# Performance work log

Hardware: AMD Instinct MI355X
Metric: run time of the kernel (lower is better)

Reference implementation:

```python
import jax, jax.numpy as jnp
import numpy as np

PROCESSING_STEPS = 3


def setup_inputs() -> dict:
    key = jax.random.key(0)
    ks = jax.random.split(key, 8)
    B, N, d = 1024, 128, 128
    y = jax.random.normal(ks[0], (B, N, d), dtype=jnp.float32)
    lengths = jax.random.randint(ks[1], (B,), 1, N + 1, dtype=jnp.int32)
    s = 0.05
    W_ih = jax.random.normal(ks[2], (4 * d, 2 * d), dtype=jnp.float32) * s
    W_hh = jax.random.normal(ks[3], (4 * d, d), dtype=jnp.float32) * s
    b_ih = jax.random.normal(ks[4], (4 * d,), dtype=jnp.float32) * s
    b_hh = jax.random.normal(ks[5], (4 * d,), dtype=jnp.float32) * s
    W_m = jax.random.normal(ks[6], (1, 2 * d), dtype=jnp.float32) * s
    b_m = jax.random.normal(ks[7], (1,), dtype=jnp.float32) * s
    mean = jnp.zeros((1,), jnp.float32)
    stddev = jnp.ones((1,), jnp.float32)
    return {"y": y, "lengths": lengths, "W_ih": W_ih, "W_hh": W_hh,
            "b_ih": b_ih, "b_hh": b_hh, "W_m": W_m, "b_m": b_m,
            "mean": mean, "stddev": stddev}


def reference(y, lengths, W_ih, W_hh, b_ih, b_hh, W_m, b_m, mean, stddev):
    # y: [B, N, d] padded atomwise representation; lengths: valid atoms per molecule
    B, N, d = y.shape
    mask = jnp.arange(N)[None, :] < lengths[:, None]          # [B, N]
    maskf = mask.astype(y.dtype)[..., None]                    # [B, N, 1]
    neg_inf = jnp.finfo(y.dtype).min

    q_star = jnp.zeros((B, 2 * d), y.dtype)
    h = jnp.zeros((B, d), y.dtype)
    c = jnp.zeros((B, d), y.dtype)

    def step(carry, _):
        q_star, h, c = carry
        # single-layer LSTM cell (PyTorch gate order i, f, g, o)
        gates = q_star @ W_ih.T + b_ih + h @ W_hh.T + b_hh     # [B, 4d]
        i, f, g, o = jnp.split(gates, 4, axis=-1)
        c2 = jax.nn.sigmoid(f) * c + jax.nn.sigmoid(i) * jnp.tanh(g)
        h2 = jax.nn.sigmoid(o) * jnp.tanh(c2)
        q = h2                                                  # [B, d]
        # attention: gather q per atom, segment softmax, scatter_add
        e = jnp.einsum('bnd,bd->bn', y, q)                      # [B, N]
        e = jnp.where(mask, e, neg_inf)
        a = jax.nn.softmax(e, axis=-1)[..., None] * maskf       # [B, N, 1]
        r = jnp.sum(a * y, axis=1)                              # [B, d]
        return (jnp.concatenate([q, r], axis=-1), h2, c2), None

    (q_star, h, c), _ = jax.lax.scan(step, (q_star, h, c), None,
                                     length=PROCESSING_STEPS)
    out = q_star @ W_m.T + b_m                                  # [B, 1]
    return out * stddev + mean
```

## Files before the change

### kernel.cpp

```cpp
#include <hip/hip_runtime.h>
#include <math.h>

#define BB 1024
#define NN 128
#define DD 128

__device__ __forceinline__ float fsig_(float x)  { return 1.0f / (1.0f + __expf(-x)); }
__device__ __forceinline__ float ftanh_(float x) { return 2.0f / (1.0f + __expf(-2.0f * x)) - 1.0f; }

__global__ __launch_bounds__(256) void k_prep2(
    const float* __restrict__ W_ih, const float* __restrict__ W_hh,
    const float* __restrict__ b_ih, const float* __restrict__ b_hh,
    float* __restrict__ Wfull, float* __restrict__ gbase) {
  int b = blockIdx.x, t = threadIdx.x;
  if (b < 64) {
    int base = b * 2048;
    for (int i = t; i < 2048; i += 256) {
      int idx = base + i;
      int j = idx >> 8, d = idx & 255;
      float v = W_ih[(j << 8) + d];
      if (d < 128) v += W_hh[(j << 7) + d];
      Wfull[idx] = v;
    }
  } else {
    __shared__ float h1l[DD];
    if (t < DD) {
      float bi = b_ih[t] + b_hh[t];
      float bg = b_ih[256 + t] + b_hh[256 + t];
      float bo = b_ih[384 + t] + b_hh[384 + t];
      float cc = fsig_(bi) * ftanh_(bg);
      h1l[t] = fsig_(bo) * ftanh_(cc);
    }
    __syncthreads();
    int j0 = (b - 64) * 128;
    if (t < 128) {
      int j = j0 + t;
      float acc = b_ih[j] + b_hh[j];
      #pragma unroll 8
      for (int d = 0; d < DD; ++d)
        acc = fmaf(W_ih[(j << 8) + d] + W_hh[(j << 7) + d], h1l[d], acc);
      gbase[j] = acc;
    }
  }
}

struct SMX {
  float ql[DD];
  float c1l[DD];
  float rp[4][DD];
  float xcat[256];
  float g2[512];
  float c2l[DD];
  float reds[4], redf[4];
};

__global__ __launch_bounds__(256, 4) void k_fused(
    const float* __restrict__ y, const int* __restrict__ lengths,
    const float* __restrict__ Wfull, const float* __restrict__ gbase,
    const float* __restrict__ b_ih, const float* __restrict__ b_hh,
    const float* __restrict__ Wm, const float* __restrict__ bm,
    const float* __restrict__ mn, const float* __restrict__ sd,
    float* __restrict__ out) {
  __shared__ SMX s;
  const int t = threadIdx.x;
  const int lane = t & 63, w = t >> 6;
  const int sub = lane & 15, g = lane >> 4;
  const int d0 = sub << 3;
  const int wbase = w << 2;
  const int m = blockIdx.x;
  const int len = lengths[m];
  const float* yb = y + (size_t)m * (NN * DD);

  if (t < DD) {
    float bi = b_ih[t] + b_hh[t];
    float bg = b_ih[256 + t] + b_hh[256 + t];
    float bo = b_ih[384 + t] + b_hh[384 + t];
    float cc = fsig_(bi) * ftanh_(bg);
    s.c1l[t] = cc;
    s.ql[t] = fsig_(bo) * ftanh_(cc);
  }

  float4 va[8], vb[8];
  #pragma unroll
  for (int it = 0; it < 8; ++it) {
    int n = (it << 4) + wbase + g;
    int nc = (n < len) ? n : (len - 1);
    const float4* yr = (const float4*)(yb + nc * DD + d0);
    va[it] = yr[0];
    vb[it] = yr[1];
  }
  __syncthreads();

  auto attn = [&](bool is_final) {
    float4 q0 = *(const float4*)&s.ql[d0];
    float4 q1 = *(const float4*)&s.ql[d0 + 4];
    float a[8], sl = 0.0f;
    #pragma unroll
    for (int it = 0; it < 8; ++it) {
      int nw = (it << 4) + wbase;
      if (nw < len) {
        int n = nw + g;
        float p = fmaf(va[it].x, q0.x, fmaf(va[it].y, q0.y,
                  fmaf(va[it].z, q0.z, fmaf(va[it].w, q0.w,
                  fmaf(vb[it].x, q1.x, fmaf(vb[it].y, q1.y,
                  fmaf(vb[it].z, q1.z, vb[it].w * q1.w)))))));
        #pragma unroll
        for (int sh = 1; sh < 16; sh <<= 1) p += __shfl_xor(p, sh, 64);
        a[it] = (n < len) ? __expf(p) : 0.0f;
      } else {
        a[it] = 0.0f;
      }
      sl += a[it];
    }
    #pragma unroll
    for (int sh = 1; sh < 64; sh <<= 1) sl += __shfl_xor(sl, sh, 64);
    if (lane == 0) s.reds[w] = sl;
    __syncthreads();
    float wscale = 16.0f / (s.reds[0] + s.reds[1] + s.reds[2] + s.reds[3]);

    float4 r0 = {0.f, 0.f, 0.f, 0.f}, r1 = {0.f, 0.f, 0.f, 0.f};
    #pragma unroll
    for (int it = 0; it < 8; ++it) {
      int nw = (it << 4) + wbase;
      if (nw < len) {
        float av = a[it];
        r0.x = fmaf(av, va[it].x, r0.x); r0.y = fmaf(av, va[it].y, r0.y);
        r0.z = fmaf(av, va[it].z, r0.z); r0.w = fmaf(av, va[it].w, r0.w);
        r1.x = fmaf(av, vb[it].x, r1.x); r1.y = fmaf(av, vb[it].y, r1.y);
        r1.z = fmaf(av, vb[it].z, r1.z); r1.w = fmaf(av, vb[it].w, r1.w);
      }
    }
    r0.x *= wscale; r0.y *= wscale; r0.z *= wscale; r0.w *= wscale;
    r1.x *= wscale; r1.y *= wscale; r1.z *= wscale; r1.w *= wscale;
    #pragma unroll
    for (int sh = 16; sh < 64; sh <<= 1) {
      r0.x += __shfl_xor(r0.x, sh, 64); r0.y += __shfl_xor(r0.y, sh, 64);
      r0.z += __shfl_xor(r0.z, sh, 64); r0.w += __shfl_xor(r0.w, sh, 64);
      r1.x += __shfl_xor(r1.x, sh, 64); r1.y += __shfl_xor(r1.y, sh, 64);
      r1.z += __shfl_xor(r1.z, sh, 64); r1.w += __shfl_xor(r1.w, sh, 64);
    }
    if (g == 0) {
      *(float4*)&s.rp[w][d0] = r0;
      *(float4*)&s.rp[w][d0 + 4] = r1;
    }
    __syncthreads();
    if (!is_final) {
      if (t < DD) s.xcat[128 + t] = s.rp[0][t] + s.rp[1][t] + s.rp[2][t] + s.rp[3][t];
      __syncthreads();
    } else {
      float part = 0.0f;
      if (t < DD) {
        float r_ = s.rp[0][t] + s.rp[1][t] + s.rp[2][t] + s.rp[3][t];
        part = Wm[t] * s.ql[t] + Wm[DD + t] * r_;
      }
      #pragma unroll
      for (int sh = 1; sh < 64; sh <<= 1) part += __shfl_xor(part, sh, 64);
      if (lane == 0) s.redf[w] = part;
      __syncthreads();
      if (t == 0)
        out[m] = (s.redf[0] + s.redf[1] + s.redf[2] + s.redf[3] + bm[0]) * sd[0] + mn[0];
    }
  };

  auto matvec = [&](int qlo, const float* bias_g, bool use_gbase) {
    #pragma unroll 4
    for (int iter = 0; iter < 32; ++iter) {
      int j = (iter << 4) + wbase + g;
      const float4* wr = (const float4*)(Wfull + (j << 8));
      float acc = 0.0f;
      #pragma unroll
      for (int q = 0; q < 4; ++q) {
        if (q < qlo) continue;
        int idx = (q << 4) + sub;
        float4 wv = wr[idx];
        float4 xa = *(const float4*)&s.xcat[idx << 2];
        acc = fmaf(wv.x, xa.x, fmaf(wv.y, xa.y, fmaf(wv.z, xa.z, fmaf(wv.w, xa.w, acc))));
      }
      #pragma unroll
      for (int sh = 1; sh < 16; sh <<= 1) acc += __shfl_xor(acc, sh, 64);
      if (sub == 0)
        s.g2[j] = acc + (use_gbase ? bias_g[j] : (b_ih[j] + b_hh[j]));
    }
  };

  auto nonlin = [&](const float* cin_src, bool save_c) {
    if (t < DD) {
      float I = s.g2[t], F = s.g2[128 + t];
      float G = s.g2[256 + t], O = s.g2[384 + t];
      float cc = fmaf(fsig_(F), cin_src[t], fsig_(I) * ftanh_(G));
      float hh = fsig_(O) * ftanh_(cc);
      if (save_c) s.c2l[t] = cc;
      s.xcat[t] = hh;
      s.ql[t] = hh;
    }
    __syncthreads();
  };

  attn(false);
  matvec(2, gbase, true);
  __syncthreads();
  nonlin(s.c1l, true);
  attn(false);
  matvec(0, nullptr, false);
  __syncthreads();
  nonlin(s.c2l, false);
  attn(true);
}

extern "C" void kernel_launch(void* const* d_in, const int* in_sizes, int n_in,
                              void* d_out, int out_size, void* d_ws, size_t ws_size,
                              hipStream_t stream) {
  const float* y    = (const float*)d_in[0];
  const int*   len  = (const int*)  d_in[1];
  const float* W_ih = (const float*)d_in[2];
  const float* W_hh = (const float*)d_in[3];
  const float* b_ih = (const float*)d_in[4];
  const float* b_hh = (const float*)d_in[5];
  const float* W_m  = (const float*)d_in[6];
  const float* b_m  = (const float*)d_in[7];
  const float* mean = (const float*)d_in[8];
  const float* sd   = (const float*)d_in[9];
  float* out = (float*)d_out;

  float* ws    = (float*)d_ws;
  float* Wfull = ws;
  float* gbase = ws + 131072;

  k_prep2<<<68, 256, 0, stream>>>(W_ih, W_hh, b_ih, b_hh, Wfull, gbase);
  k_fused<<<BB, 256, 0, stream>>>(y, len, Wfull, gbase, b_ih, b_hh,
                                  W_m, b_m, mean, sd, out);
}
```

Measured before the change: 74.99 us.

## Store fused LSTM weights as bf16 and use 512-thread blocks

The prep kernel now writes the combined LSTM weight matrix in bf16 rounding instead of fp32, halving the bytes each block streams for the gate matvec. The main kernel moves from 256 to 512 threads per block, so each wave holds fewer atom rows in registers and each thread does half the matvec rows. Reductions over waves are widened to 8 partials. This trades accuracy in the gate computation for less weight bandwidth and more parallelism per molecule.

```diff
diff --git a/kernel.cpp b/kernel.cpp
--- a/kernel.cpp
+++ b/kernel.cpp
@@ -7,11 +7,18 @@
 
 __device__ __forceinline__ float fsig_(float x)  { return 1.0f / (1.0f + __expf(-x)); }
 __device__ __forceinline__ float ftanh_(float x) { return 2.0f / (1.0f + __expf(-2.0f * x)) - 1.0f; }
-
-__global__ __launch_bounds__(256) void k_prep2(
+__device__ __forceinline__ unsigned short to_bf16_(float f) {
+  unsigned u = __float_as_uint(f);
+  u = (u + 0x7FFFu + ((u >> 16) & 1u)) >> 16;
+  return (unsigned short)u;
+}
+__device__ __forceinline__ float bf16_lo_(unsigned u) { return __uint_as_float(u << 16); }
+__device__ __forceinline__ float bf16_hi_(unsigned u) { return __uint_as_float(u & 0xFFFF0000u); }
+
+__global__ __launch_bounds__(256) void k_prep3(
     const float* __restrict__ W_ih, const float* __restrict__ W_hh,
     const float* __restrict__ b_ih, const float* __restrict__ b_hh,
-    float* __restrict__ Wfull, float* __restrict__ gbase) {
+    unsigned short* __restrict__ Wbf, float* __restrict__ gbase) {
   int b = blockIdx.x, t = threadIdx.x;
   if (b < 64) {
     int base = b * 2048;
@@ -20,7 +27,7 @@
       int j = idx >> 8, d = idx & 255;
       float v = W_ih[(j << 8) + d];
       if (d < 128) v += W_hh[(j << 7) + d];
-      Wfull[idx] = v;
+      Wbf[idx] = to_bf16_(v);
     }
   } else {
     __shared__ float h1l[DD];
@@ -47,16 +54,16 @@
 struct SMX {
   float ql[DD];
   float c1l[DD];
-  float rp[4][DD];
+  float rp[8][DD];
   float xcat[256];
   float g2[512];
   float c2l[DD];
-  float reds[4], redf[4];
+  float reds[8], redf[2];
 };
 
-__global__ __launch_bounds__(256, 4) void k_fused(
+__global__ __launch_bounds__(512, 8) void k_fused(
     const float* __restrict__ y, const int* __restrict__ lengths,
-    const float* __restrict__ Wfull, const float* __restrict__ gbase,
+    const unsigned short* __restrict__ Wbf, const float* __restrict__ gbase,
     const float* __restrict__ b_ih, const float* __restrict__ b_hh,
     const float* __restrict__ Wm, const float* __restrict__ bm,
     const float* __restrict__ mn, const float* __restrict__ sd,
@@ -66,7 +73,6 @@
   const int lane = t & 63, w = t >> 6;
   const int sub = lane & 15, g = lane >> 4;
   const int d0 = sub << 3;
-  const int wbase = w << 2;
   const int m = blockIdx.x;
   const int len = lengths[m];
   const float* yb = y + (size_t)m * (NN * DD);
@@ -80,10 +86,10 @@
     s.ql[t] = fsig_(bo) * ftanh_(cc);
   }
 
-  float4 va[8], vb[8];
+  float4 va[4], vb[4];
   #pragma unroll
-  for (int it = 0; it < 8; ++it) {
-    int n = (it << 4) + wbase + g;
+  for (int it = 0; it < 4; ++it) {
+    int n = (it << 5) + (w << 2) + g;
     int nc = (n < len) ? n : (len - 1);
     const float4* yr = (const float4*)(yb + nc * DD + d0);
     va[it] = yr[0];
@@ -94,10 +100,10 @@
   auto attn = [&](bool is_final) {
     float4 q0 = *(const float4*)&s.ql[d0];
     float4 q1 = *(const float4*)&s.ql[d0 + 4];
-    float a[8], sl = 0.0f;
-    #pragma unroll
-    for (int it = 0; it < 8; ++it) {
-      int nw = (it << 4) + wbase;
+    float a[4], sl = 0.0f;
+    #pragma unroll
+    for (int it = 0; it < 4; ++it) {
+      int nw = (it << 5) + (w << 2);
       if (nw < len) {
         int n = nw + g;
         float p = fmaf(va[it].x, q0.x, fmaf(va[it].y, q0.y,
@@ -116,12 +122,14 @@
     for (int sh = 1; sh < 64; sh <<= 1) sl += __shfl_xor(sl, sh, 64);
     if (lane == 0) s.reds[w] = sl;
     __syncthreads();
-    float wscale = 16.0f / (s.reds[0] + s.reds[1] + s.reds[2] + s.reds[3]);
+    float Z = s.reds[0] + s.reds[1] + s.reds[2] + s.reds[3] +
+              s.reds[4] + s.reds[5] + s.reds[6] + s.reds[7];
+    float wscale = 16.0f / Z;
 
     float4 r0 = {0.f, 0.f, 0.f, 0.f}, r1 = {0.f, 0.f, 0.f, 0.f};
     #pragma unroll
-    for (int it = 0; it < 8; ++it) {
-      int nw = (it << 4) + wbase;
+    for (int it = 0; it < 4; ++it) {
+      int nw = (it << 5) + (w << 2);
       if (nw < len) {
         float av = a[it];
         r0.x = fmaf(av, va[it].x, r0.x); r0.y = fmaf(av, va[it].y, r0.y);
@@ -145,41 +153,52 @@
     }
     __syncthreads();
     if (!is_final) {
-      if (t < DD) s.xcat[128 + t] = s.rp[0][t] + s.rp[1][t] + s.rp[2][t] + s.rp[3][t];
+      if (t < DD) {
+        float r_ = s.rp[0][t] + s.rp[1][t] + s.rp[2][t] + s.rp[3][t] +
+                   s.rp[4][t] + s.rp[5][t] + s.rp[6][t] + s.rp[7][t];
+        s.xcat[128 + t] = r_;
+      }
       __syncthreads();
     } else {
       float part = 0.0f;
       if (t < DD) {
-        float r_ = s.rp[0][t] + s.rp[1][t] + s.rp[2][t] + s.rp[3][t];
+        float r_ = s.rp[0][t] + s.rp[1][t] + s.rp[2][t] + s.rp[3][t] +
+                   s.rp[4][t] + s.rp[5][t] + s.rp[6][t] + s.rp[7][t];
         part = Wm[t] * s.ql[t] + Wm[DD + t] * r_;
       }
       #pragma unroll
       for (int sh = 1; sh < 64; sh <<= 1) part += __shfl_xor(part, sh, 64);
-      if (lane == 0) s.redf[w] = part;
+      if (lane == 0 && w < 2) s.redf[w] = part;
       __syncthreads();
-      if (t == 0)
-        out[m] = (s.redf[0] + s.redf[1] + s.redf[2] + s.redf[3] + bm[0]) * sd[0] + mn[0];
+      if (t == 0) out[m] = (s.redf[0] + s.redf[1] + bm[0]) * sd[0] + mn[0];
     }
   };
 
-  auto matvec = [&](int qlo, const float* bias_g, bool use_gbase) {
+  auto matvec = [&](bool r_only) {
     #pragma unroll 4
-    for (int iter = 0; iter < 32; ++iter) {
-      int j = (iter << 4) + wbase + g;
-      const float4* wr = (const float4*)(Wfull + (j << 8));
+    for (int iter = 0; iter < 16; ++iter) {
+      int j = (iter << 5) + ((t >> 6) << 2) + g;
+      const uint4* wr = (const uint4*)(Wbf + (j << 8));
       float acc = 0.0f;
       #pragma unroll
-      for (int q = 0; q < 4; ++q) {
-        if (q < qlo) continue;
-        int idx = (q << 4) + sub;
-        float4 wv = wr[idx];
-        float4 xa = *(const float4*)&s.xcat[idx << 2];
-        acc = fmaf(wv.x, xa.x, fmaf(wv.y, xa.y, fmaf(wv.z, xa.z, fmaf(wv.w, xa.w, acc))));
+      for (int q = 0; q < 2; ++q) {
+        if (r_only && q == 0) continue;
+        uint4 wv = wr[(q << 4) + sub];
+        const float4* xp = (const float4*)&s.xcat[((q << 4) + sub) << 3];
+        float4 xa = xp[0], xb = xp[1];
+        acc = fmaf(bf16_lo_(wv.x), xa.x, acc);
+        acc = fmaf(bf16_hi_(wv.x), xa.y, acc);
+        acc = fmaf(bf16_lo_(wv.y), xa.z, acc);
+        acc = fmaf(bf16_hi_(wv.y), xa.w, acc);
+        acc = fmaf(bf16_lo_(wv.z), xb.x, acc);
+        acc = fmaf(bf16_hi_(wv.z), xb.y, acc);
+        acc = fmaf(bf16_lo_(wv.w), xb.z, acc);
+        acc = fmaf(bf16_hi_(wv.w), xb.w, acc);
       }
       #pragma unroll
       for (int sh = 1; sh < 16; sh <<= 1) acc += __shfl_xor(acc, sh, 64);
       if (sub == 0)
-        s.g2[j] = acc + (use_gbase ? bias_g[j] : (b_ih[j] + b_hh[j]));
+        s.g2[j] = acc + (r_only ? gbase[j] : (b_ih[j] + b_hh[j]));
     }
   };
 
@@ -197,11 +216,11 @@
   };
 
   attn(false);
-  matvec(2, gbase, true);
+  matvec(true);
   __syncthreads();
   nonlin(s.c1l, true);
   attn(false);
-  matvec(0, nullptr, false);
+  matvec(false);
   __syncthreads();
   nonlin(s.c2l, false);
   attn(true);
@@ -222,11 +241,11 @@
   const float* sd   = (const float*)d_in[9];
   float* out = (float*)d_out;
 
-  float* ws    = (float*)d_ws;
-  float* Wfull = ws;
-  float* gbase = ws + 131072;
-
-  k_prep2<<<68, 256, 0, stream>>>(W_ih, W_hh, b_ih, b_hh, Wfull, gbase);
-  k_fused<<<BB, 256, 0, stream>>>(y, len, Wfull, gbase, b_ih, b_hh,
+  float* ws = (float*)d_ws;
+  unsigned short* Wbf = (unsigned short*)ws;
+  float* gbase = ws + 65536;
+
+  k_prep3<<<68, 256, 0, stream>>>(W_ih, W_hh, b_ih, b_hh, Wbf, gbase);
+  k_fused<<<BB, 512, 0, stream>>>(y, len, Wbf, gbase, b_ih, b_hh,
                                   W_m, b_m, mean, sd, out);
 }
```

Result: no change. 73.78 us (-1.6%).
